# Performance work log

Measured on AMD Instinct MI355X. Metric: run time of the kernel, lower is better.

Reference implementation:

```python
import jax, jax.numpy as jnp
import numpy as np

NQ, NH = 7, 4          # quantiles x horizons
G = NQ * NH            # 28 independent branches
IN_DIM, H1, H2 = 64, 64, 32


def setup_inputs() -> dict:
    key = jax.random.key(0)
    ks = jax.random.split(key, 7)
    B = 131072
    x = jax.random.normal(ks[0], (B, IN_DIM), dtype=jnp.float32)
    s1 = 1.0 / np.sqrt(IN_DIM)
    s2 = 1.0 / np.sqrt(H1)
    s3 = 1.0 / np.sqrt(H2)
    W1 = jax.random.uniform(ks[1], (G, IN_DIM, H1), jnp.float32, -s1, s1)
    b1 = jax.random.uniform(ks[2], (G, H1), jnp.float32, -s1, s1)
    W2 = jax.random.uniform(ks[3], (G, H1, H2), jnp.float32, -s2, s2)
    b2 = jax.random.uniform(ks[4], (G, H2), jnp.float32, -s2, s2)
    W3 = jax.random.uniform(ks[5], (G, H2, 1), jnp.float32, -s3, s3)
    b3 = jax.random.uniform(ks[6], (G, 1), jnp.float32, -s3, s3)
    return {"x": x, "W1": W1, "b1": b1, "W2": W2, "b2": b2, "W3": W3, "b3": b3}


def reference(x, W1, b1, W2, b2, W3, b3):
    # All G branches fused as batched GEMMs. x: [B, in]
    B = x.shape[0]
    h = jax.nn.relu(jnp.einsum('bi,gij->gbj', x, W1) + b1[:, None, :])   # [G,B,H1]
    h = jax.nn.relu(jnp.einsum('gbj,gjk->gbk', h, W2) + b2[:, None, :])  # [G,B,H2]
    o = jnp.einsum('gbk,gko->gbo', h, W3) + b3[:, None, :]               # [G,B,1]
    # branch order matches nested loop: quantile outer, horizon inner
    out = o[..., 0].reshape(NQ, NH, B).transpose(2, 0, 1)                # [B,NQ,NH]
    return out
```

## Files before the change

### kernel.cpp

```cpp
#include <hip/hip_runtime.h>
#include <hip/hip_bf16.h>
#include <hip/hip_fp16.h>

#define GN 28
#define G_TILE_BYTES 12288
#define WS_BYTES (GN * G_TILE_BYTES)

typedef __attribute__((ext_vector_type(4))) float f32x4;
typedef __attribute__((ext_vector_type(8))) short short8;
typedef _Float16 f16x8 __attribute__((ext_vector_type(8)));

__device__ __forceinline__ unsigned short f2h(float v){
  __half h = __float2half(v);
  return __builtin_bit_cast(unsigned short, h);
}
__device__ __forceinline__ f32x4 mfma16f(short8 a, short8 b, f32x4 c){
  return __builtin_amdgcn_mfma_f32_16x16x32_f16(
      __builtin_bit_cast(f16x8, a), __builtin_bit_cast(f16x8, b), c, 0, 0, 0);
}

__global__ __launch_bounds__(256) void prep_weights(
    const float* __restrict__ W1, const float* __restrict__ W2,
    unsigned char* __restrict__ ws){
  __shared__ float t1[64*65];
  __shared__ float t2[64*33];
  const int g = blockIdx.x;
  const int tid = threadIdx.x;

  {
    const f32x4* src = (const f32x4*)(W1 + g*4096);
    int k = tid >> 2, n0 = (tid & 3) * 16;
    #pragma unroll
    for (int j = 0; j < 4; ++j){
      f32x4 v = src[tid*4 + j];
      #pragma unroll
      for (int e = 0; e < 4; ++e) t1[k*65 + n0 + j*4 + e] = v[e];
    }
  }
  {
    const f32x4* src = (const f32x4*)(W2 + g*2048);
    int k = tid >> 2, n0 = (tid & 3) * 8;
    #pragma unroll
    for (int j = 0; j < 2; ++j){
      f32x4 v = src[tid*2 + j];
      #pragma unroll
      for (int e = 0; e < 4; ++e) t2[k*33 + n0 + j*4 + e] = v[e];
    }
  }
  __syncthreads();

  unsigned char* base = ws + g*G_TILE_BYTES;
  {
    int n = tid & 63, mh = tid >> 6;
    #pragma unroll
    for (int h = 0; h < 2; ++h){
      unsigned w[4];
      #pragma unroll
      for (int mm = 0; mm < 4; ++mm){
        int m = mh*8 + h*4 + mm;
        float lo = t1[(2*m    )*65 + n];
        float hi = t1[(2*m + 1)*65 + n];
        w[mm] = (unsigned)f2h(lo) | ((unsigned)f2h(hi) << 16);
      }
      int off = (n*128 + mh*32 + h*16) ^ ((n & 7) << 4);
      *(uint4*)(base + off) = make_uint4(w[0], w[1], w[2], w[3]);
    }
  }
  {
    int n2 = tid & 31, mq = tid >> 5;
    unsigned w[4];
    #pragma unroll
    for (int mm = 0; mm < 4; ++mm){
      int m = mq*4 + mm;
      int kk = 2*m;
      int ks = kk >> 5, qq = (kk >> 3) & 3, u = (kk >> 2) & 1, i = kk & 3;
      int kn = 32*ks + 16*u + 4*qq + i;
      float lo = t2[(kn    )*33 + n2];
      float hi = t2[(kn + 1)*33 + n2];
      w[mm] = (unsigned)f2h(lo) | ((unsigned)f2h(hi) << 16);
    }
    int off = (n2*128 + mq*16) ^ ((n2 & 7) << 4);
    *(uint4*)(base + 8192 + off) = make_uint4(w[0], w[1], w[2], w[3]);
  }
}

__global__ __launch_bounds__(256, 4) void mlp_fused(
    const float* __restrict__ x,  const float* __restrict__ b1,
    const float* __restrict__ b2, const float* __restrict__ W3,
    const float* __restrict__ b3, const unsigned char* __restrict__ ws,
    float* __restrict__ out){
  __shared__ uint4 wbuf[2][768];
  __shared__ float biasL[3616];

  const int tid = threadIdx.x;
  const int wv  = tid >> 6;
  const int ln  = tid & 63;
  const int l15 = ln & 15;
  const int q   = ln >> 4;
  const int rowBase = blockIdx.x * 128 + wv * 32;

  #pragma unroll
  for (int i = 0; i < 7; ++i) biasL[i*256 + tid] = b1[i*256 + tid];
  #pragma unroll
  for (int i = 0; i < 4; ++i){
    int idx = i*256 + tid;
    if (idx < 896){
      biasL[1792 + idx] = b2[idx];
      biasL[2688 + idx] = W3[idx];
    }
  }
  if (tid < 28) biasL[3584 + tid] = b3[tid];

  short8 xf[2][2];
  #pragma unroll
  for (int rt = 0; rt < 2; ++rt)
    #pragma unroll
    for (int ks = 0; ks < 2; ++ks){
      const float* p = x + (rowBase + rt*16 + l15)*64 + ks*32 + q*8;
      f32x4 a = *(const f32x4*)p;
      f32x4 b = *(const f32x4*)(p + 4);
      short8 s;
      #pragma unroll
      for (int j = 0; j < 4; ++j){
        s[j]   = (short)f2h(a[j]);
        s[4+j] = (short)f2h(b[j]);
      }
      xf[rt][ks] = s;
    }

  auto stage = [&](int g, int buf){
    const unsigned char* gb = ws + g*G_TILE_BYTES + wv*3072 + ln*16;
    uint4* lb = &wbuf[buf][wv*192];
    #pragma unroll
    for (int it = 0; it < 3; ++it){
      __builtin_amdgcn_global_load_lds(
          (const __attribute__((address_space(1))) void*)(gb + it*1024),
          (__attribute__((address_space(3))) void*)(lb + it*64), 16, 0, 0);
    }
  };

  stage(0, 0);
  asm volatile("s_waitcnt vmcnt(0)" ::: "memory");
  __syncthreads();

  for (int g = 0; g < GN; ++g){
    const int cur = g & 1;
    if (g + 1 < GN) stage(g + 1, cur ^ 1);
    const uint4* wb = wbuf[cur];

    f32x4 bias1[4], bias2[2], w3f[2];
    #pragma unroll
    for (int nt = 0; nt < 4; ++nt)
      bias1[nt] = *(const f32x4*)&biasL[g*64 + nt*16 + q*4];
    #pragma unroll
    for (int nt = 0; nt < 2; ++nt){
      bias2[nt] = *(const f32x4*)&biasL[1792 + g*32 + nt*16 + q*4];
      w3f[nt]   = *(const f32x4*)&biasL[2688 + g*32 + nt*16 + q*4];
    }
    float bias3 = biasL[3584 + g];

    short8 a1[4][2];
    #pragma unroll
    for (int nt = 0; nt < 4; ++nt)
      #pragma unroll
      for (int ks = 0; ks < 2; ++ks){
        int n = nt*16 + l15;
        int off = ((n*128 + ks*64 + q*16) ^ ((n & 7) << 4)) >> 4;
        a1[nt][ks] = __builtin_bit_cast(short8, wb[off]);
      }
    f32x4 acc1[4][2];
    #pragma unroll
    for (int nt = 0; nt < 4; ++nt)
      #pragma unroll
      for (int rt = 0; rt < 2; ++rt){
        acc1[nt][rt] = mfma16f(a1[nt][0], xf[rt][0], bias1[nt]);
        acc1[nt][rt] = mfma16f(a1[nt][1], xf[rt][1], acc1[nt][rt]);
      }

    short8 bh[2][2];
    #pragma unroll
    for (int rt = 0; rt < 2; ++rt)
      #pragma unroll
      for (int ks = 0; ks < 2; ++ks){
        f32x4 v0 = acc1[2*ks][rt], v1 = acc1[2*ks + 1][rt];
        short8 h;
        #pragma unroll
        for (int i = 0; i < 4; ++i){
          h[i]   = (short)f2h(fmaxf(v0[i], 0.0f));
          h[4+i] = (short)f2h(fmaxf(v1[i], 0.0f));
        }
        bh[rt][ks] = h;
      }

    short8 a2[2][2];
    #pragma unroll
    for (int nt = 0; nt < 2; ++nt)
      #pragma unroll
      for (int ks = 0; ks < 2; ++ks){
        int n2 = nt*16 + l15;
        int off = ((n2*128 + ks*64 + q*16) ^ ((n2 & 7) << 4)) >> 4;
        a2[nt][ks] = __builtin_bit_cast(short8, wb[512 + off]);
      }
    f32x4 acc2[2][2];
    #pragma unroll
    for (int nt = 0; nt < 2; ++nt)
      #pragma unroll
      for (int rt = 0; rt < 2; ++rt){
        acc2[nt][rt] = mfma16f(a2[nt][0], bh[rt][0], bias2[nt]);
        acc2[nt][rt] = mfma16f(a2[nt][1], bh[rt][1], acc2[nt][rt]);
      }

    #pragma unroll
    for (int rt = 0; rt < 2; ++rt){
      float p = 0.0f;
      #pragma unroll
      for (int nt = 0; nt < 2; ++nt)
        #pragma unroll
        for (int i = 0; i < 4; ++i)
          p = fmaf(fmaxf(acc2[nt][rt][i], 0.0f), w3f[nt][i], p);
      p += __shfl_xor(p, 16);
      p += __shfl_xor(p, 32);
      p += bias3;
      if (ln < 16)
        out[(rowBase + rt*16 + ln)*28 + g] = p;
    }

    asm volatile("s_waitcnt vmcnt(0)" ::: "memory");
    __syncthreads();
  }
}

extern "C" void kernel_launch(void* const* d_in, const int* in_sizes, int n_in,
                              void* d_out, int out_size, void* d_ws, size_t ws_size,
                              hipStream_t stream){
  const float* x  = (const float*)d_in[0];
  const float* W1 = (const float*)d_in[1];
  const float* b1 = (const float*)d_in[2];
  const float* W2 = (const float*)d_in[3];
  const float* b2 = (const float*)d_in[4];
  const float* W3 = (const float*)d_in[5];
  const float* b3 = (const float*)d_in[6];
  unsigned char* ws = (unsigned char*)d_ws;
  float* out = (float*)d_out;
  if (ws_size < (size_t)WS_BYTES) return;
  hipLaunchKernelGGL(prep_weights, dim3(GN), dim3(256), 0, stream, W1, W2, ws);
  hipLaunchKernelGGL(mlp_fused, dim3(1024), dim3(256), 0, stream,
                     x, b1, b2, W3, b3, ws, out);
}
```

Baseline: 147.2 us.

## Double rows per wave, halve block size, load biases from global

```diff
diff --git a/kernel.cpp b/kernel.cpp
--- a/kernel.cpp
+++ b/kernel.cpp
@@ -84,36 +84,23 @@
   }
 }
 
-__global__ __launch_bounds__(256, 4) void mlp_fused(
+__global__ __launch_bounds__(128, 2) void mlp_fused(
     const float* __restrict__ x,  const float* __restrict__ b1,
     const float* __restrict__ b2, const float* __restrict__ W3,
     const float* __restrict__ b3, const unsigned char* __restrict__ ws,
     float* __restrict__ out){
   __shared__ uint4 wbuf[2][768];
-  __shared__ float biasL[3616];
 
   const int tid = threadIdx.x;
   const int wv  = tid >> 6;
   const int ln  = tid & 63;
   const int l15 = ln & 15;
   const int q   = ln >> 4;
-  const int rowBase = blockIdx.x * 128 + wv * 32;
-
+  const int rowBase = blockIdx.x * 128 + wv * 64;
+
+  short8 xf[4][2];
   #pragma unroll
-  for (int i = 0; i < 7; ++i) biasL[i*256 + tid] = b1[i*256 + tid];
-  #pragma unroll
-  for (int i = 0; i < 4; ++i){
-    int idx = i*256 + tid;
-    if (idx < 896){
-      biasL[1792 + idx] = b2[idx];
-      biasL[2688 + idx] = W3[idx];
-    }
-  }
-  if (tid < 28) biasL[3584 + tid] = b3[tid];
-
-  short8 xf[2][2];
-  #pragma unroll
-  for (int rt = 0; rt < 2; ++rt)
+  for (int rt = 0; rt < 4; ++rt)
     #pragma unroll
     for (int ks = 0; ks < 2; ++ks){
       const float* p = x + (rowBase + rt*16 + l15)*64 + ks*32 + q*8;
@@ -129,10 +116,10 @@
     }
 
   auto stage = [&](int g, int buf){
-    const unsigned char* gb = ws + g*G_TILE_BYTES + wv*3072 + ln*16;
-    uint4* lb = &wbuf[buf][wv*192];
-    #pragma unroll
-    for (int it = 0; it < 3; ++it){
+    const unsigned char* gb = ws + g*G_TILE_BYTES + wv*6144 + ln*16;
+    uint4* lb = &wbuf[buf][wv*384];
+    #pragma unroll
+    for (int it = 0; it < 6; ++it){
       __builtin_amdgcn_global_load_lds(
           (const __attribute__((address_space(1))) void*)(gb + it*1024),
           (__attribute__((address_space(3))) void*)(lb + it*64), 16, 0, 0);
@@ -142,22 +129,24 @@
   stage(0, 0);
   asm volatile("s_waitcnt vmcnt(0)" ::: "memory");
   __syncthreads();
+
+  const f32x4 z4 = {0.f, 0.f, 0.f, 0.f};
 
   for (int g = 0; g < GN; ++g){
     const int cur = g & 1;
     if (g + 1 < GN) stage(g + 1, cur ^ 1);
     const uint4* wb = wbuf[cur];
 
-    f32x4 bias1[4], bias2[2], w3f[2];
+    f32x4 bias1v[4], bias2v[2], w3v[2];
     #pragma unroll
     for (int nt = 0; nt < 4; ++nt)
-      bias1[nt] = *(const f32x4*)&biasL[g*64 + nt*16 + q*4];
+      bias1v[nt] = *(const f32x4*)(b1 + g*64 + nt*16 + q*4);
     #pragma unroll
     for (int nt = 0; nt < 2; ++nt){
-      bias2[nt] = *(const f32x4*)&biasL[1792 + g*32 + nt*16 + q*4];
-      w3f[nt]   = *(const f32x4*)&biasL[2688 + g*32 + nt*16 + q*4];
-    }
-    float bias3 = biasL[3584 + g];
+      bias2v[nt] = *(const f32x4*)(b2 + g*32 + nt*16 + q*4);
+      w3v[nt]    = *(const f32x4*)(W3 + g*32 + nt*16 + q*4);
+    }
+    float bias3 = b3[g];
 
     short8 a1[4][2];
     #pragma unroll
@@ -168,21 +157,22 @@
         int off = ((n*128 + ks*64 + q*16) ^ ((n & 7) << 4)) >> 4;
         a1[nt][ks] = __builtin_bit_cast(short8, wb[off]);
       }
-    f32x4 acc1[4][2];
+    f32x4 acc1[4][4];
     #pragma unroll
     for (int nt = 0; nt < 4; ++nt)
       #pragma unroll
-      for (int rt = 0; rt < 2; ++rt){
-        acc1[nt][rt] = mfma16f(a1[nt][0], xf[rt][0], bias1[nt]);
+      for (int rt = 0; rt < 4; ++rt){
+        acc1[nt][rt] = mfma16f(a1[nt][0], xf[rt][0], z4);
         acc1[nt][rt] = mfma16f(a1[nt][1], xf[rt][1], acc1[nt][rt]);
       }
 
-    short8 bh[2][2];
-    #pragma unroll
-    for (int rt = 0; rt < 2; ++rt)
+    short8 bh[4][2];
+    #pragma unroll
+    for (int rt = 0; rt < 4; ++rt)
       #pragma unroll
       for (int ks = 0; ks < 2; ++ks){
-        f32x4 v0 = acc1[2*ks][rt], v1 = acc1[2*ks + 1][rt];
+        f32x4 v0 = acc1[2*ks][rt]     + bias1v[2*ks];
+        f32x4 v1 = acc1[2*ks + 1][rt] + bias1v[2*ks + 1];
         short8 h;
         #pragma unroll
         for (int i = 0; i < 4; ++i){
@@ -201,23 +191,25 @@
         int off = ((n2*128 + ks*64 + q*16) ^ ((n2 & 7) << 4)) >> 4;
         a2[nt][ks] = __builtin_bit_cast(short8, wb[512 + off]);
       }
-    f32x4 acc2[2][2];
+    f32x4 acc2[2][4];
     #pragma unroll
     for (int nt = 0; nt < 2; ++nt)
       #pragma unroll
-      for (int rt = 0; rt < 2; ++rt){
-        acc2[nt][rt] = mfma16f(a2[nt][0], bh[rt][0], bias2[nt]);
+      for (int rt = 0; rt < 4; ++rt){
+        acc2[nt][rt] = mfma16f(a2[nt][0], bh[rt][0], z4);
         acc2[nt][rt] = mfma16f(a2[nt][1], bh[rt][1], acc2[nt][rt]);
       }
 
     #pragma unroll
-    for (int rt = 0; rt < 2; ++rt){
+    for (int rt = 0; rt < 4; ++rt){
       float p = 0.0f;
       #pragma unroll
-      for (int nt = 0; nt < 2; ++nt)
+      for (int nt = 0; nt < 2; ++nt){
+        f32x4 v = acc2[nt][rt] + bias2v[nt];
         #pragma unroll
         for (int i = 0; i < 4; ++i)
-          p = fmaf(fmaxf(acc2[nt][rt][i], 0.0f), w3f[nt][i], p);
+          p = fmaf(fmaxf(v[i], 0.0f), w3v[nt][i], p);
+      }
       p += __shfl_xor(p, 16);
       p += __shfl_xor(p, 32);
       p += bias3;
@@ -244,6 +236,6 @@
   float* out = (float*)d_out;
   if (ws_size < (size_t)WS_BYTES) return;
   hipLaunchKernelGGL(prep_weights, dim3(GN), dim3(256), 0, stream, W1, W2, ws);
-  hipLaunchKernelGGL(mlp_fused, dim3(1024), dim3(256), 0, stream,
+  hipLaunchKernelGGL(mlp_fused, dim3(1024), dim3(128), 0, stream,
                      x, b1, b2, W3, b3, ws, out);
 }
```

Result: slower. 153.1 us (+4.0%).

## Stage outputs in LDS for coalesced stores, load biases from global, pack ReLU

Applied to the files above, without the earlier changes.

```diff
diff --git a/kernel.cpp b/kernel.cpp
--- a/kernel.cpp
+++ b/kernel.cpp
@@ -9,6 +9,7 @@
 typedef __attribute__((ext_vector_type(4))) float f32x4;
 typedef __attribute__((ext_vector_type(8))) short short8;
 typedef _Float16 f16x8 __attribute__((ext_vector_type(8)));
+typedef __fp16 pk16x2 __attribute__((ext_vector_type(2)));
 
 __device__ __forceinline__ unsigned short f2h(float v){
   __half h = __float2half(v);
@@ -90,7 +91,7 @@
     const float* __restrict__ b3, const unsigned char* __restrict__ ws,
     float* __restrict__ out){
   __shared__ uint4 wbuf[2][768];
-  __shared__ float biasL[3616];
+  __shared__ float outb[128*28];
 
   const int tid = threadIdx.x;
   const int wv  = tid >> 6;
@@ -99,18 +100,6 @@
   const int q   = ln >> 4;
   const int rowBase = blockIdx.x * 128 + wv * 32;
 
-  #pragma unroll
-  for (int i = 0; i < 7; ++i) biasL[i*256 + tid] = b1[i*256 + tid];
-  #pragma unroll
-  for (int i = 0; i < 4; ++i){
-    int idx = i*256 + tid;
-    if (idx < 896){
-      biasL[1792 + idx] = b2[idx];
-      biasL[2688 + idx] = W3[idx];
-    }
-  }
-  if (tid < 28) biasL[3584 + tid] = b3[tid];
-
   short8 xf[2][2];
   #pragma unroll
   for (int rt = 0; rt < 2; ++rt)
@@ -128,6 +117,22 @@
       xf[rt][ks] = s;
     }
 
+  int offA1[4][2], offA2[2][2];
+  #pragma unroll
+  for (int nt = 0; nt < 4; ++nt)
+    #pragma unroll
+    for (int ks = 0; ks < 2; ++ks){
+      int n = nt*16 + l15;
+      offA1[nt][ks] = ((n*128 + ks*64 + q*16) ^ ((n & 7) << 4)) >> 4;
+    }
+  #pragma unroll
+  for (int nt = 0; nt < 2; ++nt)
+    #pragma unroll
+    for (int ks = 0; ks < 2; ++ks){
+      int n2 = nt*16 + l15;
+      offA2[nt][ks] = (((n2*128 + ks*64 + q*16) ^ ((n2 & 7) << 4)) >> 4) + 512;
+    }
+
   auto stage = [&](int g, int buf){
     const unsigned char* gb = ws + g*G_TILE_BYTES + wv*3072 + ln*16;
     uint4* lb = &wbuf[buf][wv*192];
@@ -139,77 +144,75 @@
     }
   };
 
-  stage(0, 0);
-  asm volatile("s_waitcnt vmcnt(0)" ::: "memory");
-  __syncthreads();
-
-  for (int g = 0; g < GN; ++g){
+  auto packrelu = [&](const f32x4& v0, const f32x4& v1) -> short8 {
+    union { unsigned u[4]; short8 s; } r;
+    pk16x2 t0 = __builtin_amdgcn_cvt_pkrtz(fmaxf(v0[0],0.f), fmaxf(v0[1],0.f));
+    pk16x2 t1 = __builtin_amdgcn_cvt_pkrtz(fmaxf(v0[2],0.f), fmaxf(v0[3],0.f));
+    pk16x2 t2 = __builtin_amdgcn_cvt_pkrtz(fmaxf(v1[0],0.f), fmaxf(v1[1],0.f));
+    pk16x2 t3 = __builtin_amdgcn_cvt_pkrtz(fmaxf(v1[2],0.f), fmaxf(v1[3],0.f));
+    r.u[0] = __builtin_bit_cast(unsigned, t0);
+    r.u[1] = __builtin_bit_cast(unsigned, t1);
+    r.u[2] = __builtin_bit_cast(unsigned, t2);
+    r.u[3] = __builtin_bit_cast(unsigned, t3);
+    return r.s;
+  };
+
+  auto body = [&](int g, f32x4 (&bC)[4], f32x4 (&bN)[4]){
     const int cur = g & 1;
     if (g + 1 < GN) stage(g + 1, cur ^ 1);
+
+    const int gnext = (g + 1 < GN) ? g + 1 : GN - 1;
+    #pragma unroll
+    for (int nt = 0; nt < 4; ++nt)
+      bN[nt] = *(const f32x4*)(b1 + gnext*64 + nt*16 + q*4);
+
     const uint4* wb = wbuf[cur];
 
-    f32x4 bias1[4], bias2[2], w3f[2];
+    short8 a1[4][2];
     #pragma unroll
     for (int nt = 0; nt < 4; ++nt)
-      bias1[nt] = *(const f32x4*)&biasL[g*64 + nt*16 + q*4];
+      #pragma unroll
+      for (int ks = 0; ks < 2; ++ks)
+        a1[nt][ks] = __builtin_bit_cast(short8, wb[offA1[nt][ks]]);
+    f32x4 acc1[4][2];
+    #pragma unroll
+    for (int nt = 0; nt < 4; ++nt)
+      #pragma unroll
+      for (int rt = 0; rt < 2; ++rt){
+        acc1[nt][rt] = mfma16f(a1[nt][0], xf[rt][0], bC[nt]);
+        acc1[nt][rt] = mfma16f(a1[nt][1], xf[rt][1], acc1[nt][rt]);
+      }
+
+    f32x4 b2v[2], w3v[2];
     #pragma unroll
     for (int nt = 0; nt < 2; ++nt){
-      bias2[nt] = *(const f32x4*)&biasL[1792 + g*32 + nt*16 + q*4];
-      w3f[nt]   = *(const f32x4*)&biasL[2688 + g*32 + nt*16 + q*4];
-    }
-    float bias3 = biasL[3584 + g];
-
-    short8 a1[4][2];
-    #pragma unroll
-    for (int nt = 0; nt < 4; ++nt)
-      #pragma unroll
-      for (int ks = 0; ks < 2; ++ks){
-        int n = nt*16 + l15;
-        int off = ((n*128 + ks*64 + q*16) ^ ((n & 7) << 4)) >> 4;
-        a1[nt][ks] = __builtin_bit_cast(short8, wb[off]);
-      }
-    f32x4 acc1[4][2];
-    #pragma unroll
-    for (int nt = 0; nt < 4; ++nt)
+      b2v[nt] = *(const f32x4*)(b2 + g*32 + nt*16 + q*4);
+      w3v[nt] = *(const f32x4*)(W3 + g*32 + nt*16 + q*4);
+    }
+
+    short8 bh[2][2];
+    #pragma unroll
+    for (int rt = 0; rt < 2; ++rt)
+      #pragma unroll
+      for (int ks = 0; ks < 2; ++ks)
+        bh[rt][ks] = packrelu(acc1[2*ks][rt], acc1[2*ks + 1][rt]);
+
+    short8 a2[2][2];
+    #pragma unroll
+    for (int nt = 0; nt < 2; ++nt)
+      #pragma unroll
+      for (int ks = 0; ks < 2; ++ks)
+        a2[nt][ks] = __builtin_bit_cast(short8, wb[offA2[nt][ks]]);
+    f32x4 acc2[2][2];
+    #pragma unroll
+    for (int nt = 0; nt < 2; ++nt)
       #pragma unroll
       for (int rt = 0; rt < 2; ++rt){
-        acc1[nt][rt] = mfma16f(a1[nt][0], xf[rt][0], bias1[nt]);
-        acc1[nt][rt] = mfma16f(a1[nt][1], xf[rt][1], acc1[nt][rt]);
-      }
-
-    short8 bh[2][2];
-    #pragma unroll
-    for (int rt = 0; rt < 2; ++rt)
-      #pragma unroll
-      for (int ks = 0; ks < 2; ++ks){
-        f32x4 v0 = acc1[2*ks][rt], v1 = acc1[2*ks + 1][rt];
-        short8 h;
-        #pragma unroll
-        for (int i = 0; i < 4; ++i){
-          h[i]   = (short)f2h(fmaxf(v0[i], 0.0f));
-          h[4+i] = (short)f2h(fmaxf(v1[i], 0.0f));
-        }
-        bh[rt][ks] = h;
-      }
-
-    short8 a2[2][2];
-    #pragma unroll
-    for (int nt = 0; nt < 2; ++nt)
-      #pragma unroll
-      for (int ks = 0; ks < 2; ++ks){
-        int n2 = nt*16 + l15;
-        int off = ((n2*128 + ks*64 + q*16) ^ ((n2 & 7) << 4)) >> 4;
-        a2[nt][ks] = __builtin_bit_cast(short8, wb[512 + off]);
-      }
-    f32x4 acc2[2][2];
-    #pragma unroll
-    for (int nt = 0; nt < 2; ++nt)
-      #pragma unroll
-      for (int rt = 0; rt < 2; ++rt){
-        acc2[nt][rt] = mfma16f(a2[nt][0], bh[rt][0], bias2[nt]);
+        acc2[nt][rt] = mfma16f(a2[nt][0], bh[rt][0], b2v[nt]);
         acc2[nt][rt] = mfma16f(a2[nt][1], bh[rt][1], acc2[nt][rt]);
       }
 
+    float bias3 = b3[g];
     #pragma unroll
     for (int rt = 0; rt < 2; ++rt){
       float p = 0.0f;
@@ -217,16 +220,37 @@
       for (int nt = 0; nt < 2; ++nt)
         #pragma unroll
         for (int i = 0; i < 4; ++i)
-          p = fmaf(fmaxf(acc2[nt][rt][i], 0.0f), w3f[nt][i], p);
+          p = fmaf(fmaxf(acc2[nt][rt][i], 0.0f), w3v[nt][i], p);
       p += __shfl_xor(p, 16);
       p += __shfl_xor(p, 32);
       p += bias3;
       if (ln < 16)
-        out[(rowBase + rt*16 + ln)*28 + g] = p;
+        outb[(wv*32 + rt*16 + ln)*28 + g] = p;
     }
 
     asm volatile("s_waitcnt vmcnt(0)" ::: "memory");
     __syncthreads();
+  };
+
+  f32x4 b1A[4], b1B[4];
+  stage(0, 0);
+  #pragma unroll
+  for (int nt = 0; nt < 4; ++nt)
+    b1A[nt] = *(const f32x4*)(b1 + 0*64 + nt*16 + q*4);
+  asm volatile("s_waitcnt vmcnt(0)" ::: "memory");
+  __syncthreads();
+
+  for (int gg = 0; gg < GN; gg += 2){
+    body(gg,     b1A, b1B);
+    body(gg + 1, b1B, b1A);
+  }
+
+  const uint2* ob2 = (const uint2*)outb;
+  uint2* og2 = (uint2*)(out + blockIdx.x * (128*28));
+  #pragma unroll
+  for (int i = 0; i < 7; ++i){
+    int idx = i*256 + tid;
+    og2[idx] = ob2[idx];
   }
 }
 
```

New measurement: 144.3 us. 1.02x faster.
